# Kernel tuning notes

Measured on AMD Instinct MI355X. Metric: run time of the kernel, lower is better.

Reference implementation:

```python
import jax, jax.numpy as jnp
import numpy as np

N, T, D, H = 128, 128, 1024, 1024


def setup_inputs() -> dict:
    key = jax.random.key(0)
    k_x, k_A, k_wx, k_wh, k_wa = jax.random.split(key, 5)
    x = jax.random.normal(k_x, (N, T, D), dtype=jnp.float32)
    A = jax.random.normal(k_A, (N, H, 4, 4), dtype=jnp.float32)
    Wx = jax.random.normal(k_wx, (D, 4 * H), dtype=jnp.float32) / np.sqrt(D)
    Wh = jax.random.normal(k_wh, (H, 4 * H), dtype=jnp.float32) / np.sqrt(H)
    Wattn = jax.random.normal(k_wa, (H, 4 * H), dtype=jnp.float32) / np.sqrt(H)
    b = jnp.zeros((4 * H,), dtype=jnp.float32)
    return {"x": x, "A": A, "Wx": Wx, "Wh": Wh, "Wattn": Wattn, "b": b}


def reference(x, A, Wx, Wh, Wattn, b):
    n, h_dim = A.shape[0], A.shape[1]
    A_flat = A.reshape(n, h_dim, 16)          # (N, H, 16) spatial flattened
    h0 = A_flat.mean(axis=-1)                 # meanpool over 4x4 grid
    c0 = h0
    scale = 1.0 / np.sqrt(h_dim).astype(np.float32)

    def step(carry, x_t):
        h, c = carry
        # scaled dot-product attention over 16 spatial cells
        attn_w = jax.nn.softmax(jnp.einsum('nh,nhk->nk', h, A_flat) * scale, axis=-1)
        attn = jnp.einsum('nhk,nk->nh', A_flat, attn_w)
        a = x_t @ Wx + h @ Wh + attn @ Wattn + b   # (N, 4H)
        a_i, a_f, a_o, a_g = jnp.split(a, 4, axis=1)
        c_next = jax.nn.sigmoid(a_f) * c + jax.nn.sigmoid(a_i) * jnp.tanh(a_g)
        h_next = jax.nn.sigmoid(a_o) * jnp.tanh(c_next)
        return (h_next, c_next), h_next

    xs = jnp.transpose(x, (1, 0, 2))          # (T, N, D)
    _, hs = jax.lax.scan(step, (h0, c0), xs)  # hs: (T, N, H)
    return jnp.transpose(hs, (1, 0, 2))       # (N, T, H)
```

## Files before the change

### kernel.cpp

```cpp
#include <hip/hip_runtime.h>
#include <math.h>

#define NB 128
#define TT 128
#define HD 1024
#define FH 4096
#define QB 16
#define QSLOT (QB * 2048)

typedef __attribute__((ext_vector_type(8))) short short8v;
typedef __attribute__((ext_vector_type(4))) float float4v;

__device__ __forceinline__ ushort f2b(float f) {
    union { float f; unsigned u; } v; v.f = f;
    unsigned r = (v.u + 0x7fffu + ((v.u >> 16) & 1u)) >> 16;
    return (ushort)r;
}
__device__ __forceinline__ float b2f(ushort u) {
    union { unsigned u; float f; } v; v.u = ((unsigned)u) << 16;
    return v.f;
}
__device__ __forceinline__ float sigm(float x) { return 1.f / (1.f + __expf(-x)); }
__device__ __forceinline__ void gll16(const void* g, void* l) {
    __builtin_amdgcn_global_load_lds(
        (const __attribute__((address_space(1))) void*)g,
        (__attribute__((address_space(3))) void*)l,
        16, 0, 0);
}
__device__ __forceinline__ int swz(int c, int r) {
    return (c & 8) | ((c & 7) ^ (r & 7));
}

__global__ __launch_bounds__(256) void cvt_x(const float* __restrict__ x,
                                             ushort* __restrict__ xb) {
    size_t i = (size_t)blockIdx.x * 256 + threadIdx.x;
    const float4* p = (const float4*)x + i * 2;
    float4 va = p[0], vb = p[1];
    union { ushort u[8]; uint4 v; } o;
    o.u[0] = f2b(va.x); o.u[1] = f2b(va.y); o.u[2] = f2b(va.z); o.u[3] = f2b(va.w);
    o.u[4] = f2b(vb.x); o.u[5] = f2b(vb.y); o.u[6] = f2b(vb.z); o.u[7] = f2b(vb.w);
    ((uint4*)xb)[i] = o.v;
}

__global__ __launch_bounds__(256) void build_wt(const float* __restrict__ Wx,
                                                const float* __restrict__ Wh,
                                                const float* __restrict__ Wattn,
                                                ushort* __restrict__ WT) {
    __shared__ ushort Ls[64][65];
    int k0 = blockIdx.x * 64, n0 = blockIdx.y * 64;
    const float* W; int m;
    if (k0 < 1024)      { W = Wx;    m = 0; }
    else if (k0 < 2048) { W = Wh;    m = 1; }
    else                { W = Wattn; m = 2; }
    const int kk0 = k0 - m * 1024;
    ushort* dstm = WT + (size_t)m * FH * 1024;
    int t = threadIdx.x;
    int cc = t & 63, r4 = t >> 6;
#pragma unroll
    for (int i = 0; i < 16; ++i) {
        int r = i * 4 + r4;
        Ls[r][cc] = f2b(W[(size_t)(kk0 + r) * FH + n0 + cc]);
    }
    __syncthreads();
#pragma unroll
    for (int i = 0; i < 16; ++i) {
        int nn = i * 4 + r4;
        dstm[(size_t)(n0 + nn) * 1024 + kk0 + cc] = Ls[cc][nn];
    }
}

__global__ __launch_bounds__(256) void init_kernel(
    const float* __restrict__ Aflat, float* __restrict__ cbuf,
    ushort* __restrict__ h0buf, ushort* __restrict__ Ab16,
    float* __restrict__ qk0, float* __restrict__ qk1)
{
    __shared__ float red[4][16];
    const int n = blockIdx.x, tid = threadIdx.x;
    const int wv = tid >> 6, l = tid & 63;
    float p[16];
#pragma unroll
    for (int k = 0; k < 16; ++k) p[k] = 0.f;
#pragma unroll
    for (int u = 0; u < 4; ++u) {
        const int h = tid + u * 256;
        const size_t idx = (size_t)n * 1024 + h;
        const float4* a4 = (const float4*)(Aflat + idx * 16);
        float ar[16];
#pragma unroll
        for (int q = 0; q < 4; ++q) {
            float4 v = a4[q];
            ar[q*4+0]=v.x; ar[q*4+1]=v.y; ar[q*4+2]=v.z; ar[q*4+3]=v.w;
        }
        union { ushort us[16]; uint4 v[2]; } ob;
#pragma unroll
        for (int k = 0; k < 16; ++k) ob.us[k] = f2b(ar[k]);
        uint4* dst = (uint4*)(Ab16 + idx * 16);
        dst[0] = ob.v[0]; dst[1] = ob.v[1];

        float s = 0.f;
#pragma unroll
        for (int k = 0; k < 16; ++k) s += ar[k];
        float hv = s * 0.0625f;
        cbuf[idx] = hv;
        h0buf[idx] = f2b(hv);
#pragma unroll
        for (int k = 0; k < 16; ++k) p[k] += hv * ar[k];
    }
#pragma unroll
    for (int k = 0; k < 16; ++k) {
        float v = p[k];
        v += __shfl_xor(v, 32); v += __shfl_xor(v, 16); v += __shfl_xor(v, 8);
        v += __shfl_xor(v, 4);  v += __shfl_xor(v, 2);  v += __shfl_xor(v, 1);
        p[k] = v;
    }
    if (l == 0) {
#pragma unroll
        for (int k = 0; k < 16; ++k) red[wv][k] = p[k];
    }
    __syncthreads();
    if (tid < 16) {
        float val = red[0][tid] + red[1][tid] + red[2][tid] + red[3][tid];
#pragma unroll
        for (int bkt = 0; bkt < QB; ++bkt) {
            qk0[bkt * 2048 + n * 16 + tid] = (bkt == 0) ? val : 0.f;
            qk1[bkt * 2048 + n * 16 + tid] = 0.f;
        }
    }
}

__global__ __launch_bounds__(256) void p_gemm(
    const ushort* __restrict__ Ab16,
    const ushort* __restrict__ WatT,
    ushort* __restrict__ P2)
{
    __shared__ ushort ALDS[4 * 16 * 72];
    __shared__ ushort Bs[256 * 64];
    const int tid = threadIdx.x;
    const int wv = tid >> 6, l = tid & 63;
    const int lr = l & 15, g = l >> 4;
    const int jt = blockIdx.x, n0 = blockIdx.y * 4;
    const int snn = tid >> 6, shl = tid & 63;

    float4v acc[4][4];
#pragma unroll
    for (int i = 0; i < 4; ++i)
#pragma unroll
        for (int j = 0; j < 4; ++j) acc[i][j] = (float4v){0.f, 0.f, 0.f, 0.f};

#pragma unroll 1
    for (int kc = 0; kc < 16; ++kc) {
        __syncthreads();
        {
            const ushort* src = Ab16 + ((size_t)(n0 + snn) * 1024 + kc * 64 + shl) * 16;
            union { uint4 v[2]; ushort us[16]; } iv;
            iv.v[0] = *(const uint4*)src;
            iv.v[1] = *(const uint4*)(src + 8);
#pragma unroll
            for (int k = 0; k < 16; ++k)
                ALDS[(snn * 16 + k) * 72 + shl] = iv.us[k];
        }
#pragma unroll
        for (int i = 0; i < 8; ++i) {
            int s = i * 256 + tid;
            int r = s >> 3, c = (s & 7) ^ (r & 7);
            gll16(WatT + (size_t)(jt * 256 + r) * 1024 + kc * 64 + c * 8,
                  &Bs[s * 8]);
        }
        __syncthreads();
#pragma unroll
        for (int sub = 0; sub < 2; ++sub) {
            short8v af[4], bf[4];
#pragma unroll
            for (int nn = 0; nn < 4; ++nn)
                af[nn] = *(const short8v*)&ALDS[(nn * 16 + lr) * 72 + sub * 32 + g * 8];
#pragma unroll
            for (int nf = 0; nf < 4; ++nf) {
                int rb = wv * 64 + nf * 16 + lr;
                bf[nf] = *(const short8v*)&Bs[rb * 64 + (((sub * 4 + g) ^ (rb & 7)) * 8)];
            }
#pragma unroll
            for (int nn = 0; nn < 4; ++nn)
#pragma unroll
                for (int nf = 0; nf < 4; ++nf)
                    acc[nn][nf] = __builtin_amdgcn_mfma_f32_16x16x32_bf16(
                        af[nn], bf[nf], acc[nn][nf], 0, 0, 0);
        }
    }

#pragma unroll
    for (int nn = 0; nn < 4; ++nn)
#pragma unroll
        for (int nf = 0; nf < 4; ++nf) {
            const int j = jt * 256 + wv * 64 + nf * 16 + lr;
            union { ushort u[4]; uint2 v; } o;
#pragma unroll
            for (int jj = 0; jj < 4; ++jj) o.u[jj] = f2b(acc[nn][nf][jj]);
            *(uint2*)&P2[((size_t)(n0 + nn) * FH + j) * 16 + g * 4] = o.v;
        }
}

__global__ __launch_bounds__(256) void xa_gemm2(
    const float* __restrict__ x,
    const ushort* __restrict__ WxT,
    ushort* __restrict__ xab)
{
    __shared__ ushort As[2][128 * 64];
    __shared__ ushort Bs[2][128 * 64];
    const int tid = threadIdx.x;
    const int w = tid >> 6, l = tid & 63;
    const int wm = w >> 1, wn = w & 1;
    const int lr = l & 15, g = l >> 4;
    const int n0 = blockIdx.x * 128;
    const int mt = blockIdx.y;
    const float* Ax = x + (size_t)mt * 128 * 1024;
    const ushort* Bb = WxT + (size_t)n0 * 1024;

#define STAGEA(b, kf)                                                          \
    do {                                                                       \
        _Pragma("unroll")                                                      \
        for (int i = 0; i < 4; ++i) {                                          \
            int u = i * 256 + tid;                                             \
            int r = u >> 3, c = u & 7;                                         \
            const float* s = Ax + (size_t)r * 1024 + (kf) + c * 8;             \
            float4 v0 = *(const float4*)s;                                     \
            float4 v1 = *(const float4*)(s + 4);                               \
            union { ushort us[8]; uint4 v; } o;                                \
            o.us[0]=f2b(v0.x); o.us[1]=f2b(v0.y); o.us[2]=f2b(v0.z);           \
            o.us[3]=f2b(v0.w); o.us[4]=f2b(v1.x); o.us[5]=f2b(v1.y);           \
            o.us[6]=f2b(v1.z); o.us[7]=f2b(v1.w);                              \
            *(uint4*)&As[b][(r * 8 + (c ^ (r & 7))) * 8] = o.v;                \
        }                                                                      \
    } while (0)
#define STAGEB(b, kf)                                                          \
    do {                                                                       \
        _Pragma("unroll")                                                      \
        for (int i = 0; i < 4; ++i) {                                          \
            int s = i * 256 + tid;                                             \
            int r = s >> 3, c = s & 7;                                         \
            gll16(Bb + (size_t)r * 1024 + (kf) + (c ^ (r & 7)) * 8,            \
                  &Bs[b][s * 8]);                                              \
        }                                                                      \
    } while (0)

    float4v acc[4][4];
#pragma unroll
    for (int i = 0; i < 4; ++i)
#pragma unroll
        for (int j = 0; j < 4; ++j) acc[i][j] = (float4v){0.f, 0.f, 0.f, 0.f};

    STAGEA(0, 0);
    STAGEB(0, 0);
    __syncthreads();
    int buf = 0;
#pragma unroll 1
    for (int kc = 0; kc < 16; ++kc) {
        if (kc < 15) { STAGEA(buf ^ 1, (kc + 1) * 64); STAGEB(buf ^ 1, (kc + 1) * 64); }
        const ushort* Ab = As[buf];
        const ushort* Bbuf = Bs[buf];
#pragma unroll
        for (int sub = 0; sub < 2; ++sub) {
            short8v af[4], bf[4];
#pragma unroll
            for (int mf = 0; mf < 4; ++mf) {
                int ra = wm * 64 + mf * 16 + lr;
                af[mf] = *(const short8v*)&Ab[ra * 64 + (((sub * 4 + g) ^ (ra & 7)) * 8)];
            }
#pragma unroll
            for (int nf = 0; nf < 4; ++nf) {
                int rb = wn * 64 + nf * 16 + lr;
                bf[nf] = *(const short8v*)&Bbuf[rb * 64 + (((sub * 4 + g) ^ (rb & 7)) * 8)];
            }
#pragma unroll
            for (int mf = 0; mf < 4; ++mf)
#pragma unroll
                for (int nf = 0; nf < 4; ++nf)
                    acc[mf][nf] = __builtin_amdgcn_mfma_f32_16x16x32_bf16(
                        af[mf], bf[nf], acc[mf][nf], 0, 0, 0);
        }
        __syncthreads();
        buf ^= 1;
    }
#undef STAGEA
#undef STAGEB

#pragma unroll
    for (int mf = 0; mf < 4; ++mf)
#pragma unroll
        for (int nf = 0; nf < 4; ++nf) {
            const int col = n0 + wn * 64 + nf * 16 + lr;
#pragma unroll
            for (int j = 0; j < 4; ++j) {
                const int rl = wm * 64 + mf * 16 + g * 4 + j;
                xab[((size_t)rl * NB + mt) * FH + col] = f2b(acc[mf][nf][j]);
            }
        }
}

template <int XAF>
__global__ __launch_bounds__(256) void step_kernel(
    const ushort* __restrict__ hcur,
    ushort* __restrict__ hnext,
    const ushort* __restrict__ xb_t,
    const ushort* __restrict__ xab_t,
    const ushort* __restrict__ WxT,
    const ushort* __restrict__ WhT,
    const ushort* __restrict__ P2,
    const ushort* __restrict__ Ab16,
    const float* __restrict__ bias,
    float* __restrict__ cbuf,
    const float* __restrict__ qk_cur,
    float* __restrict__ qk_next,
    float* __restrict__ qk_zero,
    float* __restrict__ out_t)
{
    __shared__ ushort AS[16384];
    __shared__ ushort BS[16384];
    __shared__ float accL[2 * 32 * 33];
    __shared__ float wLDS[32 * 16];

    const int tid = threadIdx.x;
    const int w = tid >> 6, l = tid & 63;
    const int mh = w & 1, kh = w >> 1;
    const int lr = l & 15, g = l >> 4;

    const int bid = blockIdx.x;
    const int xcd = bid & 7, ii = bid >> 3;
    const int bx = xcd * 16 + (ii & 15);
    const int my = ii >> 4;
    const int n0 = my * 32;

    if (bid < 128) qk_zero[bid * 256 + tid] = 0.f;

    if (tid < 32) {
        const float* q = qk_cur + (n0 + tid) * 16;
        float4 s4[4];
#pragma unroll
        for (int q4 = 0; q4 < 4; ++q4) s4[q4] = ((const float4*)q)[q4];
#pragma unroll
        for (int bkt = 1; bkt < QB; ++bkt) {
            const float4* qb = (const float4*)(q + bkt * 2048);
#pragma unroll
            for (int q4 = 0; q4 < 4; ++q4) {
                float4 v = qb[q4];
                s4[q4].x += v.x; s4[q4].y += v.y; s4[q4].z += v.z; s4[q4].w += v.w;
            }
        }
        float s[16];
#pragma unroll
        for (int q4 = 0; q4 < 4; ++q4) {
            s[q4*4+0] = s4[q4].x; s[q4*4+1] = s4[q4].y;
            s[q4*4+2] = s4[q4].z; s[q4*4+3] = s4[q4].w;
        }
        float m = -1e30f;
#pragma unroll
        for (int k = 0; k < 16; ++k) { s[k] *= 0.03125f; m = fmaxf(m, s[k]); }
        float sum = 0.f;
#pragma unroll
        for (int k = 0; k < 16; ++k) { s[k] = __expf(s[k] - m); sum += s[k]; }
        float inv = 1.f / sum;
#pragma unroll
        for (int k = 0; k < 16; ++k) wLDS[tid * 16 + k] = s[k] * inv;
    }

#define STAGE(b, kc)                                                           \
    do {                                                                       \
        _Pragma("unroll")                                                      \
        for (int i = 0; i < 4; ++i) {                                          \
            int u = i * 256 + tid;                                             \
            int skh = u >> 9, rem = u & 511;                                   \
            int r = rem >> 4, c = rem & 15;                                    \
            int lc = swz(c, r);                                                \
            const ushort* src;                                                 \
            if (XAF == 1)                                                      \
                src = hcur + (size_t)(n0 + r) * 1024 + skh * 512               \
                      + (kc) * 128 + lc * 8;                                   \
            else                                                               \
                src = skh                                                      \
                    ? hcur + (size_t)(n0 + r) * 1024 + (kc) * 128 + lc * 8     \
                    : xb_t + (size_t)(n0 + r) * (TT * HD) + (kc) * 128 + lc * 8;\
            gll16(src, AS + (((b) * 2 + skh) * 512 + rem) * 8);                \
        }                                                                      \
        _Pragma("unroll")                                                      \
        for (int i = 0; i < 4; ++i) {                                          \
            int u = i * 256 + tid;                                             \
            int skh = u >> 9, rem = u & 511;                                   \
            int r = rem >> 4, c = rem & 15;                                    \
            int lc = swz(c, r);                                                \
            int jg = (r >> 3) * 1024 + bx * 8 + (r & 7);                       \
            const ushort* src;                                                 \
            if (XAF == 1)                                                      \
                src = WhT + (size_t)jg * 1024 + skh * 512 + (kc) * 128 + lc * 8;\
            else                                                               \
                src = (skh ? WhT : WxT) + (size_t)jg * 1024                    \
                      + (kc) * 128 + lc * 8;                                   \
            gll16(src, BS + (((b) * 2 + skh) * 512 + rem) * 8);                \
        }                                                                      \
    } while (0)

    float4v acc[2];
    acc[0] = (float4v){0.f, 0.f, 0.f, 0.f};
    acc[1] = (float4v){0.f, 0.f, 0.f, 0.f};

    const int NK = (XAF == 1) ? 4 : 8;
    STAGE(0, 0);
    __syncthreads();
    int buf = 0;
#pragma unroll 1
    for (int kc = 0; kc < NK; ++kc) {
        if (kc + 1 < NK) STAGE(buf ^ 1, kc + 1);
        const int base = (buf * 2 + kh) * 512;
        const int ra = mh * 16 + lr;
#pragma unroll
        for (int ks = 0; ks < 4; ++ks) {
            const int c = ks * 4 + g;
            short8v af = *(const short8v*)&AS[(base + ra * 16 + swz(c, ra)) * 8];
#pragma unroll
            for (int nf = 0; nf < 2; ++nf) {
                const int rb = nf * 16 + lr;
                short8v bf = *(const short8v*)&BS[(base + rb * 16 + swz(c, rb)) * 8];
                acc[nf] = __builtin_amdgcn_mfma_f32_16x16x32_bf16(af, bf, acc[nf], 0, 0, 0);
            }
        }
        __syncthreads();
        buf ^= 1;
    }
#undef STAGE

#pragma unroll
    for (int nf = 0; nf < 2; ++nf)
#pragma unroll
        for (int jj = 0; jj < 4; ++jj)
            accL[(kh * 32 + mh * 16 + g * 4 + jj) * 33 + nf * 16 + lr] = acc[nf][jj];
    __syncthreads();

    const int n_l = tid >> 3, hcl = tid & 7;
    const int n = n0 + n_l;
    const int hc = bx * 8 + hcl;

    float wv_[16];
#pragma unroll
    for (int k = 0; k < 16; ++k) wv_[k] = wLDS[n_l * 16 + k];

    float val[4];
#pragma unroll
    for (int q = 0; q < 4; ++q) {
        const int cq = q * 8 + hcl;
        float v = accL[n_l * 33 + cq] + accL[(32 + n_l) * 33 + cq]
                + bias[q * 1024 + hc];
        if (XAF == 1) v += b2f(xab_t[(size_t)n * FH + q * 1024 + hc]);
        const ushort* pp = P2 + ((size_t)n * FH + q * 1024 + hc) * 16;
        union { uint4 v[2]; ushort us[16]; } pv;
        pv.v[0] = *(const uint4*)pp;
        pv.v[1] = *(const uint4*)(pp + 8);
#pragma unroll
        for (int k = 0; k < 16; ++k) v += wv_[k] * b2f(pv.us[k]);
        val[q] = v;
    }

    const size_t chidx = (size_t)n * 1024 + hc;
    float cn = sigm(val[1]) * cbuf[chidx] + sigm(val[0]) * tanhf(val[3]);
    float hv = sigm(val[2]) * tanhf(cn);
    cbuf[chidx] = cn;
    out_t[(size_t)n * (TT * HD) + hc] = hv;
    hnext[chidx] = f2b(hv);

    union { uint4 v[2]; ushort us[16]; } av;
    {
        const ushort* ap = Ab16 + chidx * 16;
        av.v[0] = *(const uint4*)ap;
        av.v[1] = *(const uint4*)(ap + 8);
    }
    float vv[16];
#pragma unroll
    for (int k = 0; k < 16; ++k) vv[k] = hv * b2f(av.us[k]);
    {
        bool hi = (hcl & 1);
#pragma unroll
        for (int q = 0; q < 8; ++q) {
            float send = hi ? vv[q] : vv[q + 8];
            float recv = __shfl_xor(send, 1);
            vv[q] = (hi ? vv[q + 8] : vv[q]) + recv;
        }
        hi = (hcl & 2);
#pragma unroll
        for (int q = 0; q < 4; ++q) {
            float send = hi ? vv[q] : vv[q + 4];
            float recv = __shfl_xor(send, 2);
            vv[q] = (hi ? vv[q + 4] : vv[q]) + recv;
        }
        hi = (hcl & 4);
#pragma unroll
        for (int q = 0; q < 2; ++q) {
            float send = hi ? vv[q] : vv[q + 2];
            float recv = __shfl_xor(send, 4);
            vv[q] = (hi ? vv[q + 2] : vv[q]) + recv;
        }
    }
    const int kbase = ((hcl & 1) << 3) | ((hcl & 2) << 1) | ((hcl & 4) >> 1);
    float* qdst = qk_next + (bx & (QB - 1)) * 2048 + n * 16;
    atomicAdd(qdst + kbase,     vv[0]);
    atomicAdd(qdst + kbase + 1, vv[1]);
}

extern "C" void kernel_launch(void* const* d_in, const int* in_sizes, int n_in,
                              void* d_out, int out_size, void* d_ws, size_t ws_size,
                              hipStream_t stream) {
    const float* x     = (const float*)d_in[0];
    const float* A     = (const float*)d_in[1];
    const float* Wx    = (const float*)d_in[2];
    const float* Wh    = (const float*)d_in[3];
    const float* Wattn = (const float*)d_in[4];
    const float* b     = (const float*)d_in[5];
    float* out = (float*)d_out;

    ushort* WT   = (ushort*)d_ws;
    ushort* WxT  = WT;
    ushort* WhT  = WT + (size_t)FH * 1024;
    ushort* WatT = WT + (size_t)2 * FH * 1024;
    ushort* Ab16 = WT + (size_t)3 * FH * 1024;
    ushort* hb   = Ab16 + (size_t)NB * HD * 16;
    float*  cb   = (float*)(hb + (size_t)2 * NB * HD);
    float*  qk   = cb + (size_t)NB * HD;
    ushort* P2   = (ushort*)(qk + 3 * QSLOT);
    ushort* tail = P2 + (size_t)NB * FH * 16;

    const size_t base  = (size_t)((char*)tail - (char*)d_ws);
    const size_t xasz  = (size_t)TT * NB * FH * 2;
    const size_t xbsz  = (size_t)NB * TT * HD * 2;

    build_wt<<<dim3(48, 64), 256, 0, stream>>>(Wx, Wh, Wattn, WT);
    init_kernel<<<NB, 256, 0, stream>>>(A, cb, hb, Ab16, qk, qk + QSLOT);
    p_gemm<<<dim3(16, 32), 256, 0, stream>>>(Ab16, WatT, P2);

    if (ws_size >= base + xasz) {
        ushort* xab = tail;
        xa_gemm2<<<dim3(32, 128), 256, 0, stream>>>(x, WxT, xab);
        for (int t = 0; t < TT; ++t) {
            const ushort* hc = hb + (size_t)(t & 1) * NB * HD;
            ushort* hn       = hb + (size_t)((t + 1) & 1) * NB * HD;
            const float* qc  = qk + (size_t)(t % 3) * QSLOT;
            float* qn        = qk + (size_t)((t + 1) % 3) * QSLOT;
            float* qz        = qk + (size_t)((t + 2) % 3) * QSLOT;
            step_kernel<1><<<512, 256, 0, stream>>>(
                hc, hn, nullptr, xab + (size_t)t * NB * FH, WxT, WhT, P2, Ab16,
                b, cb, qc, qn, qz, out + (size_t)t * HD);
        }
    } else {
        ushort* xb = tail;
        cvt_x<<<8192, 256, 0, stream>>>(x, xb);
        for (int t = 0; t < TT; ++t) {
            const ushort* hc = hb + (size_t)(t & 1) * NB * HD;
            ushort* hn       = hb + (size_t)((t + 1) & 1) * NB * HD;
            const float* qc  = qk + (size_t)(t % 3) * QSLOT;
            float* qn        = qk + (size_t)((t + 1) % 3) * QSLOT;
            float* qz        = qk + (size_t)((t + 2) % 3) * QSLOT;
            step_kernel<0><<<512, 256, 0, stream>>>(
                hc, hn, xb + (size_t)t * HD, nullptr, WxT, WhT, P2, Ab16,
                b, cb, qc, qn, qz, out + (size_t)t * HD);
        }
    }
}
```

Measured before the change: 1.737 ms.

## Restructure recurrent step kernel to load full h tile once and stream Wh from global

Adds a new per-timestep kernel that loads the block's whole 32x1024 bf16 h slice into LDS in one go, reads Wh fragments directly from global memory into registers, and splits K across four waves whose partial sums are reduced through LDS. This replaces the double-buffered staged loop and is meant to cut synchronisation and pipeline overhead on the latency-bound recurrent step. It also remaps the xa GEMM grid to group tiles per XCD and swaps sigmoid/tanh for fast reciprocal-based approximations, which slightly lowers numerical accuracy.

```diff
diff --git a/kernel.cpp b/kernel.cpp
--- a/kernel.cpp
+++ b/kernel.cpp
@@ -20,7 +20,12 @@
     union { unsigned u; float f; } v; v.u = ((unsigned)u) << 16;
     return v.f;
 }
-__device__ __forceinline__ float sigm(float x) { return 1.f / (1.f + __expf(-x)); }
+__device__ __forceinline__ float sigm(float x) {
+    return __builtin_amdgcn_rcpf(1.f + __expf(-x));
+}
+__device__ __forceinline__ float tanh_fast(float x) {
+    return 1.f - 2.f * __builtin_amdgcn_rcpf(1.f + __expf(2.f * x));
+}
 __device__ __forceinline__ void gll16(const void* g, void* l) {
     __builtin_amdgcn_global_load_lds(
         (const __attribute__((address_space(1))) void*)g,
@@ -199,7 +204,7 @@
         }
 }
 
-__global__ __launch_bounds__(256) void xa_gemm2(
+__global__ __launch_bounds__(256) void xa_gemm3(
     const float* __restrict__ x,
     const ushort* __restrict__ WxT,
     ushort* __restrict__ xab)
@@ -210,9 +215,13 @@
     const int w = tid >> 6, l = tid & 63;
     const int wm = w >> 1, wn = w & 1;
     const int lr = l & 15, g = l >> 4;
-    const int n0 = blockIdx.x * 128;
-    const int mt = blockIdx.y;
-    const float* Ax = x + (size_t)mt * 128 * 1024;
+
+    const int bid = blockIdx.x;
+    const int xcd = bid & 7, ii = bid >> 3;
+    const int mt = xcd * 16 + (ii & 15);
+    const int n0 = (ii >> 4) * 128;
+
+    const float*  Ax = x + (size_t)mt * 128 * 1024;
     const ushort* Bb = WxT + (size_t)n0 * 1024;
 
 #define STAGEA(b, kf)                                                          \
@@ -234,8 +243,8 @@
 #define STAGEB(b, kf)                                                          \
     do {                                                                       \
         _Pragma("unroll")                                                      \
-        for (int i = 0; i < 4; ++i) {                                          \
-            int s = i * 256 + tid;                                             \
+        for (int s2 = 0; s2 < 4; ++s2) {                                       \
+            int s = s2 * 256 + tid;                                            \
             int r = s >> 3, c = s & 7;                                         \
             gll16(Bb + (size_t)r * 1024 + (kf) + (c ^ (r & 7)) * 8,            \
                   &Bs[b][s * 8]);                                              \
@@ -296,12 +305,201 @@
         }
 }
 
-template <int XAF>
-__global__ __launch_bounds__(256) void step_kernel(
+__global__ __launch_bounds__(256) void step_kernel2(
+    const ushort* __restrict__ hcur,
+    ushort* __restrict__ hnext,
+    const ushort* __restrict__ xab_t,
+    const ushort* __restrict__ WhT,
+    const ushort* __restrict__ P2,
+    const ushort* __restrict__ Ab16,
+    const float* __restrict__ bias,
+    float* __restrict__ cbuf,
+    const float* __restrict__ qk_cur,
+    float* __restrict__ qk_next,
+    float* __restrict__ qk_zero,
+    float* __restrict__ out_t)
+{
+    __shared__ ushort AS[32768];
+    __shared__ float wLDS[32 * 16];
+    float* accL = (float*)AS;
+
+    const int tid = threadIdx.x;
+    const int w = tid >> 6, l = tid & 63;
+    const int lr = l & 15, g = l >> 4;
+
+    const int bid = blockIdx.x;
+    const int xcd = bid & 7, ii = bid >> 3;
+    const int bx = xcd * 16 + (ii & 15);
+    const int my = ii >> 4;
+    const int n0 = my * 32;
+
+#pragma unroll
+    for (int i = 0; i < 16; ++i) {
+        int u = i * 256 + tid;
+        int r = u >> 7, c = u & 127;
+        int lc = (c & ~7) | ((c ^ r) & 7);
+        gll16(hcur + (size_t)(n0 + r) * 1024 + lc * 8, AS + u * 8);
+    }
+
+    if (bid < 128) qk_zero[bid * 256 + tid] = 0.f;
+
+    if (tid < 32) {
+        const float* q = qk_cur + (n0 + tid) * 16;
+        float4 s4[4];
+#pragma unroll
+        for (int q4 = 0; q4 < 4; ++q4) s4[q4] = ((const float4*)q)[q4];
+#pragma unroll
+        for (int bkt = 1; bkt < QB; ++bkt) {
+            const float4* qb = (const float4*)(q + bkt * 2048);
+#pragma unroll
+            for (int q4 = 0; q4 < 4; ++q4) {
+                float4 v = qb[q4];
+                s4[q4].x += v.x; s4[q4].y += v.y; s4[q4].z += v.z; s4[q4].w += v.w;
+            }
+        }
+        float s[16];
+#pragma unroll
+        for (int q4 = 0; q4 < 4; ++q4) {
+            s[q4*4+0] = s4[q4].x; s[q4*4+1] = s4[q4].y;
+            s[q4*4+2] = s4[q4].z; s[q4*4+3] = s4[q4].w;
+        }
+        float m = -1e30f;
+#pragma unroll
+        for (int k = 0; k < 16; ++k) { s[k] *= 0.03125f; m = fmaxf(m, s[k]); }
+        float sum = 0.f;
+#pragma unroll
+        for (int k = 0; k < 16; ++k) { s[k] = __expf(s[k] - m); sum += s[k]; }
+        float inv = __builtin_amdgcn_rcpf(sum);
+#pragma unroll
+        for (int k = 0; k < 16; ++k) wLDS[tid * 16 + k] = s[k] * inv;
+    }
+
+    __syncthreads();
+
+    float4v acc[2][2];
+#pragma unroll
+    for (int i = 0; i < 2; ++i)
+#pragma unroll
+        for (int j = 0; j < 2; ++j) acc[i][j] = (float4v){0.f, 0.f, 0.f, 0.f};
+
+    {
+        const int kq = w;
+        const ushort* bp[2];
+#pragma unroll
+        for (int nf = 0; nf < 2; ++nf) {
+            int rb = nf * 16 + lr;
+            int jg = (rb >> 3) * 1024 + bx * 8 + (rb & 7);
+            bp[nf] = WhT + (size_t)jg * 1024 + kq * 256 + g * 8;
+        }
+#pragma unroll
+        for (int s = 0; s < 8; ++s) {
+            short8v b0 = *(const short8v*)(bp[0] + s * 32);
+            short8v b1 = *(const short8v*)(bp[1] + s * 32);
+            const int c = kq * 32 + s * 4 + g;
+            short8v a0, a1;
+            {
+                int ra = lr;
+                int slot = (c & ~7) | ((c ^ ra) & 7);
+                a0 = *(const short8v*)&AS[(ra * 128 + slot) * 8];
+            }
+            {
+                int ra = 16 + lr;
+                int slot = (c & ~7) | ((c ^ ra) & 7);
+                a1 = *(const short8v*)&AS[(ra * 128 + slot) * 8];
+            }
+            acc[0][0] = __builtin_amdgcn_mfma_f32_16x16x32_bf16(a0, b0, acc[0][0], 0, 0, 0);
+            acc[0][1] = __builtin_amdgcn_mfma_f32_16x16x32_bf16(a0, b1, acc[0][1], 0, 0, 0);
+            acc[1][0] = __builtin_amdgcn_mfma_f32_16x16x32_bf16(a1, b0, acc[1][0], 0, 0, 0);
+            acc[1][1] = __builtin_amdgcn_mfma_f32_16x16x32_bf16(a1, b1, acc[1][1], 0, 0, 0);
+        }
+    }
+
+    __syncthreads();
+
+#pragma unroll
+    for (int mf = 0; mf < 2; ++mf)
+#pragma unroll
+        for (int nf = 0; nf < 2; ++nf)
+#pragma unroll
+            for (int j = 0; j < 4; ++j)
+                accL[(w * 32 + mf * 16 + g * 4 + j) * 33 + nf * 16 + lr]
+                    = acc[mf][nf][j];
+    __syncthreads();
+
+    const int n_l = tid >> 3, hcl = tid & 7;
+    const int n = n0 + n_l;
+    const int hc = bx * 8 + hcl;
+
+    float wv_[16];
+#pragma unroll
+    for (int k = 0; k < 16; ++k) wv_[k] = wLDS[n_l * 16 + k];
+
+    float val[4];
+#pragma unroll
+    for (int q = 0; q < 4; ++q) {
+        const int cq = q * 8 + hcl;
+        float v = bias[q * 1024 + hc]
+                + accL[(0 * 32 + n_l) * 33 + cq] + accL[(1 * 32 + n_l) * 33 + cq]
+                + accL[(2 * 32 + n_l) * 33 + cq] + accL[(3 * 32 + n_l) * 33 + cq];
+        v += b2f(xab_t[(size_t)n * FH + q * 1024 + hc]);
+        const ushort* pp = P2 + ((size_t)n * FH + q * 1024 + hc) * 16;
+        union { uint4 v[2]; ushort us[16]; } pv;
+        pv.v[0] = *(const uint4*)pp;
+        pv.v[1] = *(const uint4*)(pp + 8);
+#pragma unroll
+        for (int k = 0; k < 16; ++k) v += wv_[k] * b2f(pv.us[k]);
+        val[q] = v;
+    }
+
+    const size_t chidx = (size_t)n * 1024 + hc;
+    float cn = sigm(val[1]) * cbuf[chidx] + sigm(val[0]) * tanh_fast(val[3]);
+    float hv = sigm(val[2]) * tanh_fast(cn);
+    cbuf[chidx] = cn;
+    out_t[(size_t)n * (TT * HD) + hc] = hv;
+    hnext[chidx] = f2b(hv);
+
+    union { uint4 v[2]; ushort us[16]; } av;
+    {
+        const ushort* ap = Ab16 + chidx * 16;
+        av.v[0] = *(const uint4*)ap;
+        av.v[1] = *(const uint4*)(ap + 8);
+    }
+    float vv[16];
+#pragma unroll
+    for (int k = 0; k < 16; ++k) vv[k] = hv * b2f(av.us[k]);
+    {
+        bool hi = (hcl & 1);
+#pragma unroll
+        for (int q = 0; q < 8; ++q) {
+            float send = hi ? vv[q] : vv[q + 8];
+            float recv = __shfl_xor(send, 1);
+            vv[q] = (hi ? vv[q + 8] : vv[q]) + recv;
+        }
+        hi = (hcl & 2);
+#pragma unroll
+        for (int q = 0; q < 4; ++q) {
+            float send = hi ? vv[q] : vv[q + 4];
+            float recv = __shfl_xor(send, 2);
+            vv[q] = (hi ? vv[q + 4] : vv[q]) + recv;
+        }
+        hi = (hcl & 4);
+#pragma unroll
+        for (int q = 0; q < 2; ++q) {
+            float send = hi ? vv[q] : vv[q + 2];
+            float recv = __shfl_xor(send, 4);
+            vv[q] = (hi ? vv[q + 2] : vv[q]) + recv;
+        }
+    }
+    const int kbase = ((hcl & 1) << 3) | ((hcl & 2) << 1) | ((hcl & 4) >> 1);
+    float* qdst = qk_next + (bx & (QB - 1)) * 2048 + n * 16;
+    atomicAdd(qdst + kbase,     vv[0]);
+    atomicAdd(qdst + kbase + 1, vv[1]);
+}
+
+__global__ __launch_bounds__(256) void step_kernel0(
     const ushort* __restrict__ hcur,
     ushort* __restrict__ hnext,
     const ushort* __restrict__ xb_t,
-    const ushort* __restrict__ xab_t,
     const ushort* __restrict__ WxT,
     const ushort* __restrict__ WhT,
     const ushort* __restrict__ P2,
@@ -329,39 +527,6 @@
     const int my = ii >> 4;
     const int n0 = my * 32;
 
-    if (bid < 128) qk_zero[bid * 256 + tid] = 0.f;
-
-    if (tid < 32) {
-        const float* q = qk_cur + (n0 + tid) * 16;
-        float4 s4[4];
-#pragma unroll
-        for (int q4 = 0; q4 < 4; ++q4) s4[q4] = ((const float4*)q)[q4];
-#pragma unroll
-        for (int bkt = 1; bkt < QB; ++bkt) {
-            const float4* qb = (const float4*)(q + bkt * 2048);
-#pragma unroll
-            for (int q4 = 0; q4 < 4; ++q4) {
-                float4 v = qb[q4];
-                s4[q4].x += v.x; s4[q4].y += v.y; s4[q4].z += v.z; s4[q4].w += v.w;
-            }
-        }
-        float s[16];
-#pragma unroll
-        for (int q4 = 0; q4 < 4; ++q4) {
-            s[q4*4+0] = s4[q4].x; s[q4*4+1] = s4[q4].y;
-            s[q4*4+2] = s4[q4].z; s[q4*4+3] = s4[q4].w;
-        }
-        float m = -1e30f;
-#pragma unroll
-        for (int k = 0; k < 16; ++k) { s[k] *= 0.03125f; m = fmaxf(m, s[k]); }
-        float sum = 0.f;
-#pragma unroll
-        for (int k = 0; k < 16; ++k) { s[k] = __expf(s[k] - m); sum += s[k]; }
-        float inv = 1.f / sum;
-#pragma unroll
-        for (int k = 0; k < 16; ++k) wLDS[tid * 16 + k] = s[k] * inv;
-    }
-
 #define STAGE(b, kc)                                                           \
     do {                                                                       \
         _Pragma("unroll")                                                      \
@@ -370,14 +535,9 @@
             int skh = u >> 9, rem = u & 511;                                   \
             int r = rem >> 4, c = rem & 15;                                    \
             int lc = swz(c, r);                                                \
-            const ushort* src;                                                 \
-            if (XAF == 1)                                                      \
-                src = hcur + (size_t)(n0 + r) * 1024 + skh * 512               \
-                      + (kc) * 128 + lc * 8;                                   \
-            else                                                               \
-                src = skh                                                      \
-                    ? hcur + (size_t)(n0 + r) * 1024 + (kc) * 128 + lc * 8     \
-                    : xb_t + (size_t)(n0 + r) * (TT * HD) + (kc) * 128 + lc * 8;\
+            const ushort* src = skh                                            \
+                ? hcur + (size_t)(n0 + r) * 1024 + (kc) * 128 + lc * 8         \
+                : xb_t + (size_t)(n0 + r) * (TT * HD) + (kc) * 128 + lc * 8;   \
             gll16(src, AS + (((b) * 2 + skh) * 512 + rem) * 8);                \
         }                                                                      \
         _Pragma("unroll")                                                      \
@@ -387,27 +547,56 @@
             int r = rem >> 4, c = rem & 15;                                    \
             int lc = swz(c, r);                                                \
             int jg = (r >> 3) * 1024 + bx * 8 + (r & 7);                       \
-            const ushort* src;                                                 \
-            if (XAF == 1)                                                      \
-                src = WhT + (size_t)jg * 1024 + skh * 512 + (kc) * 128 + lc * 8;\
-            else                                                               \
-                src = (skh ? WhT : WxT) + (size_t)jg * 1024                    \
-                      + (kc) * 128 + lc * 8;                                   \
+            const ushort* src = (skh ? WhT : WxT) + (size_t)jg * 1024          \
+                                + (kc) * 128 + lc * 8;                         \
             gll16(src, BS + (((b) * 2 + skh) * 512 + rem) * 8);                \
         }                                                                      \
     } while (0)
 
+    STAGE(0, 0);
+
+    if (bid < 128) qk_zero[bid * 256 + tid] = 0.f;
+
+    if (tid < 32) {
+        const float* q = qk_cur + (n0 + tid) * 16;
+        float4 s4[4];
+#pragma unroll
+        for (int q4 = 0; q4 < 4; ++q4) s4[q4] = ((const float4*)q)[q4];
+#pragma unroll
+        for (int bkt = 1; bkt < QB; ++bkt) {
+            const float4* qb = (const float4*)(q + bkt * 2048);
+#pragma unroll
+            for (int q4 = 0; q4 < 4; ++q4) {
+                float4 v = qb[q4];
+                s4[q4].x += v.x; s4[q4].y += v.y; s4[q4].z += v.z; s4[q4].w += v.w;
+            }
+        }
+        float s[16];
+#pragma unroll
+        for (int q4 = 0; q4 < 4; ++q4) {
+            s[q4*4+0] = s4[q4].x; s[q4*4+1] = s4[q4].y;
+            s[q4*4+2] = s4[q4].z; s[q4*4+3] = s4[q4].w;
+        }
+        float m = -1e30f;
+#pragma unroll
+        for (int k = 0; k < 16; ++k) { s[k] *= 0.03125f; m = fmaxf(m, s[k]); }
+        float sum = 0.f;
+#pragma unroll
+        for (int k = 0; k < 16; ++k) { s[k] = __expf(s[k] - m); sum += s[k]; }
+        float inv = __builtin_amdgcn_rcpf(sum);
+#pragma unroll
+        for (int k = 0; k < 16; ++k) wLDS[tid * 16 + k] = s[k] * inv;
+    }
+
     float4v acc[2];
     acc[0] = (float4v){0.f, 0.f, 0.f, 0.f};
     acc[1] = (float4v){0.f, 0.f, 0.f, 0.f};
 
-    const int NK = (XAF == 1) ? 4 : 8;
-    STAGE(0, 0);
     __syncthreads();
     int buf = 0;
 #pragma unroll 1
-    for (int kc = 0; kc < NK; ++kc) {
-        if (kc + 1 < NK) STAGE(buf ^ 1, kc + 1);
+    for (int kc = 0; kc < 8; ++kc) {
+        if (kc + 1 < 8) STAGE(buf ^ 1, kc + 1);
         const int base = (buf * 2 + kh) * 512;
         const int ra = mh * 16 + lr;
 #pragma unroll
@@ -447,7 +636,6 @@
         const int cq = q * 8 + hcl;
         float v = accL[n_l * 33 + cq] + accL[(32 + n_l) * 33 + cq]
                 + bias[q * 1024 + hc];
-        if (XAF == 1) v += b2f(xab_t[(size_t)n * FH + q * 1024 + hc]);
         const ushort* pp = P2 + ((size_t)n * FH + q * 1024 + hc) * 16;
         union { uint4 v[2]; ushort us[16]; } pv;
         pv.v[0] = *(const uint4*)pp;
@@ -458,8 +646,8 @@
     }
 
     const size_t chidx = (size_t)n * 1024 + hc;
-    float cn = sigm(val[1]) * cbuf[chidx] + sigm(val[0]) * tanhf(val[3]);
-    float hv = sigm(val[2]) * tanhf(cn);
+    float cn = sigm(val[1]) * cbuf[chidx] + sigm(val[0]) * tanh_fast(val[3]);
+    float hv = sigm(val[2]) * tanh_fast(cn);
     cbuf[chidx] = cn;
     out_t[(size_t)n * (TT * HD) + hc] = hv;
     hnext[chidx] = f2b(hv);
@@ -534,15 +722,15 @@
 
     if (ws_size >= base + xasz) {
         ushort* xab = tail;
-        xa_gemm2<<<dim3(32, 128), 256, 0, stream>>>(x, WxT, xab);
+        xa_gemm3<<<4096, 256, 0, stream>>>(x, WxT, xab);
         for (int t = 0; t < TT; ++t) {
             const ushort* hc = hb + (size_t)(t & 1) * NB * HD;
             ushort* hn       = hb + (size_t)((t + 1) & 1) * NB * HD;
             const float* qc  = qk + (size_t)(t % 3) * QSLOT;
             float* qn        = qk + (size_t)((t + 1) % 3) * QSLOT;
             float* qz        = qk + (size_t)((t + 2) % 3) * QSLOT;
-            step_kernel<1><<<512, 256, 0, stream>>>(
-                hc, hn, nullptr, xab + (size_t)t * NB * FH, WxT, WhT, P2, Ab16,
+            step_kernel2<<<512, 256, 0, stream>>>(
+                hc, hn, xab + (size_t)t * NB * FH, WhT, P2, Ab16,
                 b, cb, qc, qn, qz, out + (size_t)t * HD);
         }
     } else {
@@ -554,8 +742,8 @@
             const float* qc  = qk + (size_t)(t % 3) * QSLOT;
             float* qn        = qk + (size_t)((t + 1) % 3) * QSLOT;
             float* qz        = qk + (size_t)((t + 2) % 3) * QSLOT;
-            step_kernel<0><<<512, 256, 0, stream>>>(
-                hc, hn, xb + (size_t)t * HD, nullptr, WxT, WhT, P2, Ab16,
+            step_kernel0<<<512, 256, 0, stream>>>(
+                hc, hn, xb + (size_t)t * HD, WxT, WhT, P2, Ab16,
                 b, cb, qc, qn, qz, out + (size_t)t * HD);
         }
     }
```

Measured after the change: 1.820 ms. +4.8%, slower.
